# Optimization experiments

Measured on AMD Instinct MI355X. Metric: run time of the kernel, lower is better.

## Reference

```python
import jax, jax.numpy as jnp
import numpy as np

N = 50000      # nodes
E = 600000     # edges (avg degree 12)
IN = 128       # in_feat
HID = IN // 2  # 64
OUT = 128      # out_feat (must equal in_feat, see msg_linear)

# NOTE: the torch source uses nn.LeakyReLU(True): the positional arg is
# negative_slope, so slope == 1.0 (identity). We reproduce that faithfully.
NEG_SLOPE = 1.0

def leaky(v):
    return jnp.where(v >= 0, v, NEG_SLOPE * v)

def _linear_params(key, fan_in, fan_out):
    kw, kb = jax.random.split(key)
    bound = 1.0 / np.sqrt(fan_in)
    W = jax.random.uniform(kw, (fan_in, fan_out), jnp.float32, -bound, bound)
    b = jax.random.uniform(kb, (fan_out,), jnp.float32, -bound, bound)
    return W, b

def setup_inputs() -> dict:
    key = jax.random.key(0)
    ks = jax.random.split(key, 10)
    x = jax.random.normal(ks[0], (N, IN), jnp.float32)
    e = jax.random.normal(ks[1], (E, IN), jnp.float32)
    src = jax.random.randint(ks[2], (E,), 0, N, jnp.int64)
    dst = jax.random.randint(ks[3], (E,), 0, N, jnp.int64)
    W_nl1, b_nl1 = _linear_params(ks[4], IN, HID)    # node_linear1
    W_el, b_el = _linear_params(ks[5], IN, HID)      # edge_linear
    W1, b1 = _linear_params(ks[6], HID, HID)         # node_mlp layer 1
    W2, b2 = _linear_params(ks[7], HID, OUT)         # node_mlp layer 2
    W_nl2, b_nl2 = _linear_params(ks[8], IN, HID)    # node_linear2
    km, ke = jax.random.split(ks[9])
    W_ml, b_ml = _linear_params(km, IN, HID)         # msg_linear (in_feat==out_feat)
    W_em, b_em = _linear_params(ke, HID, OUT)        # edge_mlp layer
    return dict(x=x, e=e, src=src, dst=dst,
                W_nl1=W_nl1, b_nl1=b_nl1, W_el=W_el, b_el=b_el,
                W1=W1, b1=b1, W2=W2, b2=b2,
                W_nl2=W_nl2, b_nl2=b_nl2, W_ml=W_ml, b_ml=b_ml,
                W_em=W_em, b_em=b_em)

def reference(x, e, src, dst,
              W_nl1, b_nl1, W_el, b_el,
              W1, b1, W2, b2,
              W_nl2, b_nl2, W_ml, b_ml,
              W_em, b_em):
    # apply_edges: e' = node_mlp(node_linear1(x[src]) + edge_linear(e))
    z = x[src] @ W_nl1 + b_nl1 + e @ W_el + b_el            # [E, HID]
    e_new = leaky(leaky(z) @ W1 + b1) @ W2 + b2             # [E, OUT]
    # update_all(copy_e, sum): scatter-sum edge messages to destination nodes
    msg = jax.ops.segment_sum(e_new, dst, num_segments=N)   # [N, OUT]
    # x' = edge_mlp(node_linear2(x) + msg_linear(msg))
    h = leaky(x @ W_nl2 + b_nl2 + msg @ W_ml + b_ml)        # [N, HID]
    return h @ W_em + b_em                                  # [N, OUT]
```

## Files before the change

### kernel.cpp

```cpp
#include <hip/hip_runtime.h>

#define N_NODES 50000
#define N_EDGES 600000

typedef float v2f __attribute__((ext_vector_type(2)));

#define WF_PA   0
#define WF_UN   6400000
#define WI_CNT   9600000
#define WI_OFF   9650000
#define WI_CUR   9700000
#define WI_BSUM  9750000
#define WI_BOFF  9750256
#define WI_EPAIR 9750512
#define WF_T2   10950528
#define WF_BEG  10954624
#define WF_RH   10954752
#define WF_K1   10954816
#define WF_WAX  10958912
#define WF_WE   10975296
#define WF_R    10983488
#define WF_C2   10983616

#define NBLK_SCAN 196
#define NBLK_E    2344
#define NBLK_PT2  17
#define NBLK_K1   16
#define NBLK_WA   97
#define NBLK_PXA  391

__global__ __launch_bounds__(256) void f1_pret2_zero(
        const float* __restrict__ W2, const float* __restrict__ W_ml,
        const float* __restrict__ b1, const float* __restrict__ b2,
        float* __restrict__ T2, float* __restrict__ be_g,
        int* __restrict__ cnt) {
    int bid = blockIdx.x;
    if (bid < NBLK_PT2) {
        int idx = bid * 256 + threadIdx.x;
        if (idx < 4096) {
            int i = idx >> 6, j = idx & 63;
            float s = 0.f;
            for (int k = 0; k < 128; ++k) s += W2[i*128+k] * W_ml[k*64+j];
            T2[idx] = s;
        } else if (idx < 4224) {
            int j = idx - 4096;
            float s = b2[j];
            for (int k = 0; k < 64; ++k) s += b1[k] * W2[k*128+j];
            be_g[j] = s;
        }
    } else {
        int i = (bid - NBLK_PT2) * 256 + threadIdx.x;
        if (i < N_NODES) cnt[i] = 0;
    }
}

__global__ __launch_bounds__(256) void f2_prek1_hist(
        const float* __restrict__ W1, const float* __restrict__ T2,
        float* __restrict__ K1,
        const int* __restrict__ dst, int* __restrict__ cnt) {
    int bid = blockIdx.x;
    if (bid < NBLK_K1) {
        int idx = bid * 256 + threadIdx.x;
        int i = idx >> 6, j = idx & 63;
        float s = 0.f;
        for (int k = 0; k < 64; ++k) s += W1[i*64+k] * T2[k*64+j];
        K1[idx] = s;
    } else {
        int e = (bid - NBLK_K1) * 256 + threadIdx.x;
        if (e < N_EDGES) atomicAdd(&cnt[dst[e]], 1);
    }
}

__global__ __launch_bounds__(256) void f3_prewa_scana(
        const float* __restrict__ W_nl1, const float* __restrict__ W_el,
        const float* __restrict__ W_nl2, const float* __restrict__ K1,
        const float* __restrict__ b_nl1, const float* __restrict__ b_el,
        const float* __restrict__ be_g, const float* __restrict__ W_ml,
        float* __restrict__ WAX, float* __restrict__ WE,
        float* __restrict__ rh_g,
        const int* __restrict__ cnt, int* __restrict__ bsum) {
    int bid = blockIdx.x;
    if (bid < NBLK_WA) {
        int idx = bid * 256 + threadIdx.x;
        if (idx < 16384) {
            int i = idx >> 7, j = idx & 127;
            if (j < 64) {
                WAX[idx] = W_nl2[i*64+j];
            } else {
                float s = 0.f;
                for (int k = 0; k < 64; ++k) s += W_nl1[i*64+k] * K1[k*64+(j-64)];
                WAX[idx] = s;
            }
        } else if (idx < 24576) {
            int p = idx - 16384; int i = p >> 6, j = p & 63;
            float s = 0.f;
            for (int k = 0; k < 64; ++k) s += W_el[i*64+k] * K1[k*64+j];
            WE[p] = s;
        } else if (idx < 24640) {
            int t = idx - 24576;
            float s = 0.f;
            for (int k = 0; k < 64; ++k)  s += (b_nl1[k] + b_el[k]) * K1[k*64+t];
            for (int k = 0; k < 128; ++k) s += be_g[k] * W_ml[k*64+t];
            rh_g[t] = s;
        }
    } else {
        __shared__ int s[256];
        int blk = bid - NBLK_WA;
        int i = blk * 256 + threadIdx.x;
        int v = (i < N_NODES) ? cnt[i] : 0;
        s[threadIdx.x] = v;
        __syncthreads();
        for (int d = 128; d > 0; d >>= 1) {
            if (threadIdx.x < d) s[threadIdx.x] += s[threadIdx.x + d];
            __syncthreads();
        }
        if (threadIdx.x == 0) bsum[blk] = s[0];
    }
}

__global__ __launch_bounds__(256) void f4_prerc_scanb(
        const float* __restrict__ rh_g, const float* __restrict__ W_em,
        const float* __restrict__ b_nl2, const float* __restrict__ b_ml,
        const float* __restrict__ b_em,
        float* __restrict__ r, float* __restrict__ c2,
        const int* __restrict__ bsum, int* __restrict__ boff) {
    int t = threadIdx.x;
    if (blockIdx.x == 0) {
        if (t < 128) {
            float s = 0.f;
            for (int k = 0; k < 64; ++k) s += rh_g[k] * W_em[k*128+t];
            r[t] = s;
        } else {
            int j = t - 128;
            float s = b_em[j];
            for (int k = 0; k < 64; ++k) s += (b_nl2[k] + b_ml[k]) * W_em[k*128+j];
            c2[j] = s;
        }
    } else {
        __shared__ int s[256];
        int v = (t < NBLK_SCAN) ? bsum[t] : 0;
        s[t] = v;
        __syncthreads();
        for (int d = 1; d < 256; d <<= 1) {
            int tv = (t >= d) ? s[t - d] : 0;
            __syncthreads();
            s[t] += tv;
            __syncthreads();
        }
        if (t < NBLK_SCAN) boff[t] = s[t] - v;
    }
}

__global__ __launch_bounds__(256) void scan_c_kernel(const int* __restrict__ cnt,
                                                     const int* __restrict__ boff,
                                                     int* __restrict__ offs,
                                                     int* __restrict__ cursor) {
    __shared__ int s[256];
    int i = blockIdx.x * 256 + threadIdx.x;
    int t = threadIdx.x;
    int v = (i < N_NODES) ? cnt[i] : 0;
    s[t] = v;
    __syncthreads();
    for (int d = 1; d < 256; d <<= 1) {
        int tv = (t >= d) ? s[t - d] : 0;
        __syncthreads();
        s[t] += tv;
        __syncthreads();
    }
    if (i < N_NODES) {
        int ex = s[t] - v + boff[blockIdx.x];
        offs[i] = ex;
        cursor[i] = ex;
    }
}

__global__ __launch_bounds__(256) void f5_fill_pxa(
        const int* __restrict__ dst, const int* __restrict__ src,
        int* __restrict__ cursor, int2* __restrict__ epair,
        const float* __restrict__ x, const float* __restrict__ WAX,
        float* __restrict__ PA) {
    int bid = blockIdx.x;
    if (bid < NBLK_E) {
        int e = bid * 256 + threadIdx.x;
        if (e < N_EDGES) {
            int pos = atomicAdd(&cursor[dst[e]], 1);
            epair[pos] = make_int2(e, src[e]);
        }
        return;
    }
    __shared__ float As[32][133];
    __shared__ float Ws[32][128];
    int base = (bid - NBLK_E) * 128;
    int t = threadIdx.x;
    int cg = t & 15, rg = t >> 4;
    int c0 = cg * 8, r0 = rg * 8;

    float acc[8][8];
    #pragma unroll
    for (int i = 0; i < 8; ++i)
        #pragma unroll
        for (int j = 0; j < 8; ++j) acc[i][j] = 0.f;

    int arow0 = t >> 3;
    int akq   = t & 7;

    for (int k0 = 0; k0 < 128; k0 += 32) {
        __syncthreads();
        #pragma unroll
        for (int i = 0; i < 4; ++i) {
            int row = arow0 + i * 32;
            int n = base + row;
            float4 v = make_float4(0.f, 0.f, 0.f, 0.f);
            if (n < N_NODES)
                v = *(const float4*)&x[(size_t)n * 128 + k0 + akq * 4];
            As[akq * 4 + 0][row] = v.x;
            As[akq * 4 + 1][row] = v.y;
            As[akq * 4 + 2][row] = v.z;
            As[akq * 4 + 3][row] = v.w;
        }
        #pragma unroll
        for (int i = 0; i < 4; ++i) {
            int idx = t + i * 256;
            int row = idx >> 5, q4 = idx & 31;
            *(float4*)&Ws[row][q4 * 4] =
                *(const float4*)&WAX[(size_t)(k0 + row) * 128 + q4 * 4];
        }
        __syncthreads();
        #pragma unroll 8
        for (int k = 0; k < 32; ++k) {
            float a[8], w[8];
            *(float4*)&a[0] = *(const float4*)&As[k][r0];
            *(float4*)&a[4] = *(const float4*)&As[k][r0 + 4];
            *(float4*)&w[0] = *(const float4*)&Ws[k][c0];
            *(float4*)&w[4] = *(const float4*)&Ws[k][c0 + 4];
            #pragma unroll
            for (int i = 0; i < 8; ++i)
                #pragma unroll
                for (int jj = 0; jj < 8; ++jj)
                    acc[i][jj] += a[i] * w[jj];
        }
    }

    #pragma unroll
    for (int i = 0; i < 8; ++i) {
        int n = base + r0 + i;
        if (n < N_NODES) {
            *(float4*)&PA[(size_t)n * 128 + c0]     = *(float4*)&acc[i][0];
            *(float4*)&PA[(size_t)n * 128 + c0 + 4] = *(float4*)&acc[i][4];
        }
    }
}

__global__ __launch_bounds__(256) void gather_kernel(
        const float* __restrict__ PA, const float* __restrict__ ef,
        const int* __restrict__ cnt, const int* __restrict__ offs,
        const int2* __restrict__ epair, const float* __restrict__ WE,
        float* __restrict__ u) {
    int n    = (int)((blockIdx.x * 256 + threadIdx.x) >> 6);
    int lane = threadIdx.x & 63;
    if (n >= N_NODES) return;
    int off = offs[n], deg = cnt[n];
    int col2 = lane * 2;
    float a_val = PA[(size_t)n * 128 + lane];
    float apx = 0.f, ae0 = 0.f, ae1 = 0.f;
    for (int c0 = 0; c0 < deg; c0 += 64) {
        int j = c0 + lane;
        int2 p = make_int2(0, 0);
        if (j < deg) p = epair[off + j];
        int m = deg - c0; if (m > 64) m = 64;
        for (int j2 = 0; j2 < m; j2 += 8) {
            float xv[8]; v2f ev[8]; float msk[8];
            #pragma unroll
            for (int uu = 0; uu < 8; ++uu) {
                int jj = j2 + uu;
                int idx = (jj < m) ? jj : (m - 1);
                msk[uu] = (jj < m) ? 1.f : 0.f;
                int e_ = __shfl(p.x, idx);
                int s_ = __shfl(p.y, idx);
                xv[uu] = PA[(size_t)s_ * 128 + 64 + lane];
                ev[uu] = __builtin_nontemporal_load(
                            (const v2f*)(ef + (size_t)e_ * 128 + col2));
            }
            #pragma unroll
            for (int uu = 0; uu < 8; ++uu) {
                apx += msk[uu] * xv[uu];
                ae0 += msk[uu] * ev[uu][0];
                ae1 += msk[uu] * ev[uu][1];
            }
        }
    }
    const float* WEl = WE + lane;
    float pr0 = 0.f, pr1 = 0.f, pr2 = 0.f, pr3 = 0.f;
    for (int k0 = 0; k0 < 128; k0 += 8) {
        float wv[8], evv[8];
        #pragma unroll
        for (int uu = 0; uu < 8; ++uu) {
            int kk = k0 + uu;
            wv[uu]  = WEl[kk * 64];
            evv[uu] = __shfl((kk & 1) ? ae1 : ae0, kk >> 1);
        }
        pr0 += evv[0]*wv[0] + evv[4]*wv[4];
        pr1 += evv[1]*wv[1] + evv[5]*wv[5];
        pr2 += evv[2]*wv[2] + evv[6]*wv[6];
        pr3 += evv[3]*wv[3] + evv[7]*wv[7];
    }
    u[(size_t)n * 64 + lane] = a_val + apx + ((pr0 + pr1) + (pr2 + pr3));
}

__global__ __launch_bounds__(256) void gemm2_kernel(
        const float* __restrict__ u, const int* __restrict__ cnt,
        const float* __restrict__ W_em,
        const float* __restrict__ rvec, const float* __restrict__ c2,
        float* __restrict__ out) {
    __shared__ float UsT[64][69];
    __shared__ float Wem[64][128];
    int base = blockIdx.x * 64;
    int t = threadIdx.x;
    int cg = t & 15, rg = t >> 4;
    int c0 = cg * 8, r0 = rg * 4;

    #pragma unroll
    for (int i = 0; i < 4; ++i) {
        int idx = t + i * 256;
        int row = idx >> 4, kq = idx & 15;
        int n = base + row;
        float4 v = make_float4(0.f, 0.f, 0.f, 0.f);
        if (n < N_NODES) v = *(const float4*)&u[(size_t)n * 64 + kq * 4];
        UsT[kq * 4 + 0][row] = v.x;
        UsT[kq * 4 + 1][row] = v.y;
        UsT[kq * 4 + 2][row] = v.z;
        UsT[kq * 4 + 3][row] = v.w;
    }
    #pragma unroll
    for (int i = 0; i < 8; ++i) {
        int idx = t + i * 256;
        int row = idx >> 5, q4 = idx & 31;
        *(float4*)&Wem[row][q4 * 4] = *(const float4*)&W_em[(size_t)row * 128 + q4 * 4];
    }

    float4 rva = *(const float4*)&rvec[c0];
    float4 rvb = *(const float4*)&rvec[c0 + 4];
    float4 cva = *(const float4*)&c2[c0];
    float4 cvb = *(const float4*)&c2[c0 + 4];
    float acc[4][8];
    #pragma unroll
    for (int i = 0; i < 4; ++i) {
        int n = base + r0 + i;
        float dg = (n < N_NODES) ? (float)cnt[n] : 0.f;
        acc[i][0] = cva.x + dg * rva.x;  acc[i][1] = cva.y + dg * rva.y;
        acc[i][2] = cva.z + dg * rva.z;  acc[i][3] = cva.w + dg * rva.w;
        acc[i][4] = cvb.x + dg * rvb.x;  acc[i][5] = cvb.y + dg * rvb.y;
        acc[i][6] = cvb.z + dg * rvb.z;  acc[i][7] = cvb.w + dg * rvb.w;
    }
    __syncthreads();

    #pragma unroll 8
    for (int k = 0; k < 64; ++k) {
        float a[4], w[8];
        *(float4*)&a[0] = *(const float4*)&UsT[k][r0];
        *(float4*)&w[0] = *(const float4*)&Wem[k][c0];
        *(float4*)&w[4] = *(const float4*)&Wem[k][c0 + 4];
        #pragma unroll
        for (int i = 0; i < 4; ++i)
            #pragma unroll
            for (int j = 0; j < 8; ++j)
                acc[i][j] += a[i] * w[j];
    }

    #pragma unroll
    for (int i = 0; i < 4; ++i) {
        int n = base + r0 + i;
        if (n < N_NODES) {
            *(float4*)&out[(size_t)n * 128 + c0]     = *(float4*)&acc[i][0];
            *(float4*)&out[(size_t)n * 128 + c0 + 4] = *(float4*)&acc[i][4];
        }
    }
}

extern "C" void kernel_launch(void* const* d_in, const int* in_sizes, int n_in,
                              void* d_out, int out_size, void* d_ws, size_t ws_size,
                              hipStream_t stream) {
    const float* x     = (const float*)d_in[0];
    const float* ef    = (const float*)d_in[1];
    const int*   src   = (const int*)d_in[2];
    const int*   dst   = (const int*)d_in[3];
    const float* W_nl1 = (const float*)d_in[4];
    const float* b_nl1 = (const float*)d_in[5];
    const float* W_el  = (const float*)d_in[6];
    const float* b_el  = (const float*)d_in[7];
    const float* W1    = (const float*)d_in[8];
    const float* b1    = (const float*)d_in[9];
    const float* W2    = (const float*)d_in[10];
    const float* b2    = (const float*)d_in[11];
    const float* W_nl2 = (const float*)d_in[12];
    const float* b_nl2 = (const float*)d_in[13];
    const float* W_ml  = (const float*)d_in[14];
    const float* b_ml  = (const float*)d_in[15];
    const float* W_em  = (const float*)d_in[16];
    const float* b_em  = (const float*)d_in[17];

    int*   wsI = (int*)d_ws;
    float* wsF = (float*)d_ws;
    float* PA     = wsF + WF_PA;
    float* uN     = wsF + WF_UN;
    int*   cnt    = wsI + WI_CNT;
    int*   offs   = wsI + WI_OFF;
    int*   cursor = wsI + WI_CUR;
    int*   bsum   = wsI + WI_BSUM;
    int*   boff   = wsI + WI_BOFF;
    int2*  epair  = (int2*)(wsI + WI_EPAIR);
    float* T2   = wsF + WF_T2;
    float* be_g = wsF + WF_BEG;
    float* rh_g = wsF + WF_RH;
    float* K1   = wsF + WF_K1;
    float* WAX  = wsF + WF_WAX;
    float* WE   = wsF + WF_WE;
    float* r    = wsF + WF_R;
    float* c2   = wsF + WF_C2;

    f1_pret2_zero<<<NBLK_PT2 + NBLK_SCAN, 256, 0, stream>>>(
        W2, W_ml, b1, b2, T2, be_g, cnt);
    f2_prek1_hist<<<NBLK_K1 + NBLK_E, 256, 0, stream>>>(
        W1, T2, K1, dst, cnt);
    f3_prewa_scana<<<NBLK_WA + NBLK_SCAN, 256, 0, stream>>>(
        W_nl1, W_el, W_nl2, K1, b_nl1, b_el, be_g, W_ml, WAX, WE, rh_g,
        cnt, bsum);
    f4_prerc_scanb<<<2, 256, 0, stream>>>(
        rh_g, W_em, b_nl2, b_ml, b_em, r, c2, bsum, boff);
    scan_c_kernel<<<NBLK_SCAN, 256, 0, stream>>>(cnt, boff, offs, cursor);
    f5_fill_pxa<<<NBLK_E + NBLK_PXA, 256, 0, stream>>>(
        dst, src, cursor, epair, x, WAX, PA);

    gather_kernel<<<(N_NODES + 3) / 4, 256, 0, stream>>>(
        PA, ef, cnt, offs, epair, WE, uN);

    gemm2_kernel<<<(N_NODES + 63) / 64, 256, 0, stream>>>(
        uN, cnt, W_em, r, c2, (float*)d_out);
}
```

Baseline: 281.6 us.

## Move per-node WE projection out of gather into a tiled GEMM fused with output GEMM

The gather kernel now only sums edge features (as float4 loads split across two half-waves, each handling alternate edges) and projected source features. It writes the raw 128-wide edge sum and the partial node value to the workspace. The per-node 128x64 WE projection, previously done with shuffles and uncoalesced weight loads inside each wavefront, moves into a shared-memory tiled GEMM that is fused ahead of the existing W_em GEMM. This removes shuffle-heavy per-node matvec work from the latency-bound gather, at the cost of an extra 50000x128 intermediate written and read back through global memory.

Result: faster. 271.1 us (-3.7%).

```diff
diff --git a/kernel.cpp b/kernel.cpp
--- a/kernel.cpp
+++ b/kernel.cpp
@@ -4,30 +4,32 @@
 #define N_EDGES 600000
 
 typedef float v2f __attribute__((ext_vector_type(2)));
-
-#define WF_PA   0
-#define WF_UN   6400000
-#define WI_CNT   9600000
-#define WI_OFF   9650000
-#define WI_CUR   9700000
-#define WI_BSUM  9750000
-#define WI_BOFF  9750256
-#define WI_EPAIR 9750512
-#define WF_T2   10950528
-#define WF_BEG  10954624
-#define WF_RH   10954752
-#define WF_K1   10954816
-#define WF_WAX  10958912
-#define WF_WE   10975296
-#define WF_R    10983488
-#define WF_C2   10983616
+typedef float v4f __attribute__((ext_vector_type(4)));
+
+#define WF_PA    0
+#define WF_ES    6400000
+#define WF_UP    12800000
+#define WI_CNT   16000000
+#define WI_OFF   16050000
+#define WI_CUR   16100000
+#define WI_BSUM  16150000
+#define WI_BOFF  16150256
+#define WI_EPAIR 16150512
+#define WF_T2    17350528
+#define WF_BEG   17354624
+#define WF_RH    17354752
+#define WF_K1    17354816
+#define WF_WAX   17358912
+#define WF_WE    17375296
+#define WF_R     17383488
+#define WF_C2    17383616
 
 #define NBLK_SCAN 196
 #define NBLK_E    2344
 #define NBLK_PT2  17
 #define NBLK_K1   16
 #define NBLK_WA   97
-#define NBLK_PXA  391
+#define NBLK_PA   391
 
 __global__ __launch_bounds__(256) void f1_pret2_zero(
         const float* __restrict__ W2, const float* __restrict__ W_ml,
@@ -174,7 +176,7 @@
     }
 }
 
-__global__ __launch_bounds__(256) void f5_fill_pxa(
+__global__ __launch_bounds__(256) void f5_fill_pa(
         const int* __restrict__ dst, const int* __restrict__ src,
         int* __restrict__ cursor, int2* __restrict__ epair,
         const float* __restrict__ x, const float* __restrict__ WAX,
@@ -254,125 +256,171 @@
 __global__ __launch_bounds__(256) void gather_kernel(
         const float* __restrict__ PA, const float* __restrict__ ef,
         const int* __restrict__ cnt, const int* __restrict__ offs,
-        const int2* __restrict__ epair, const float* __restrict__ WE,
-        float* __restrict__ u) {
+        const int2* __restrict__ epair,
+        float* __restrict__ es, float* __restrict__ u_part) {
     int n    = (int)((blockIdx.x * 256 + threadIdx.x) >> 6);
     int lane = threadIdx.x & 63;
     if (n >= N_NODES) return;
     int off = offs[n], deg = cnt[n];
-    int col2 = lane * 2;
-    float a_val = PA[(size_t)n * 128 + lane];
-    float apx = 0.f, ae0 = 0.f, ae1 = 0.f;
+    int half = lane >> 5;
+    int hl   = lane & 31;
+    int ce4  = hl * 4;
+    int cp2  = hl * 2;
+    float ae0 = 0.f, ae1 = 0.f, ae2 = 0.f, ae3 = 0.f;
+    float ap0 = 0.f, ap1 = 0.f;
     for (int c0 = 0; c0 < deg; c0 += 64) {
         int j = c0 + lane;
         int2 p = make_int2(0, 0);
         if (j < deg) p = epair[off + j];
         int m = deg - c0; if (m > 64) m = 64;
         for (int j2 = 0; j2 < m; j2 += 8) {
-            float xv[8]; v2f ev[8]; float msk[8];
+            v4f ev[4]; v2f pv[4]; float msk[4];
             #pragma unroll
-            for (int uu = 0; uu < 8; ++uu) {
-                int jj = j2 + uu;
+            for (int q = 0; q < 4; ++q) {
+                int jj = j2 + q * 2 + half;
                 int idx = (jj < m) ? jj : (m - 1);
-                msk[uu] = (jj < m) ? 1.f : 0.f;
+                msk[q] = (jj < m) ? 1.f : 0.f;
                 int e_ = __shfl(p.x, idx);
                 int s_ = __shfl(p.y, idx);
-                xv[uu] = PA[(size_t)s_ * 128 + 64 + lane];
-                ev[uu] = __builtin_nontemporal_load(
-                            (const v2f*)(ef + (size_t)e_ * 128 + col2));
+                ev[q] = __builtin_nontemporal_load(
+                            (const v4f*)(ef + (size_t)e_ * 128 + ce4));
+                pv[q] = *(const v2f*)(PA + (size_t)s_ * 128 + 64 + cp2);
             }
             #pragma unroll
-            for (int uu = 0; uu < 8; ++uu) {
-                apx += msk[uu] * xv[uu];
-                ae0 += msk[uu] * ev[uu][0];
-                ae1 += msk[uu] * ev[uu][1];
+            for (int q = 0; q < 4; ++q) {
+                ae0 += msk[q] * ev[q][0];
+                ae1 += msk[q] * ev[q][1];
+                ae2 += msk[q] * ev[q][2];
+                ae3 += msk[q] * ev[q][3];
+                ap0 += msk[q] * pv[q][0];
+                ap1 += msk[q] * pv[q][1];
             }
         }
     }
-    const float* WEl = WE + lane;
-    float pr0 = 0.f, pr1 = 0.f, pr2 = 0.f, pr3 = 0.f;
-    for (int k0 = 0; k0 < 128; k0 += 8) {
-        float wv[8], evv[8];
-        #pragma unroll
-        for (int uu = 0; uu < 8; ++uu) {
-            int kk = k0 + uu;
-            wv[uu]  = WEl[kk * 64];
-            evv[uu] = __shfl((kk & 1) ? ae1 : ae0, kk >> 1);
-        }
-        pr0 += evv[0]*wv[0] + evv[4]*wv[4];
-        pr1 += evv[1]*wv[1] + evv[5]*wv[5];
-        pr2 += evv[2]*wv[2] + evv[6]*wv[6];
-        pr3 += evv[3]*wv[3] + evv[7]*wv[7];
-    }
-    u[(size_t)n * 64 + lane] = a_val + apx + ((pr0 + pr1) + (pr2 + pr3));
-}
-
-__global__ __launch_bounds__(256) void gemm2_kernel(
-        const float* __restrict__ u, const int* __restrict__ cnt,
+    ae0 += __shfl_xor(ae0, 32);
+    ae1 += __shfl_xor(ae1, 32);
+    ae2 += __shfl_xor(ae2, 32);
+    ae3 += __shfl_xor(ae3, 32);
+    ap0 += __shfl_xor(ap0, 32);
+    ap1 += __shfl_xor(ap1, 32);
+    if (half == 0) {
+        *(float4*)&es[(size_t)n * 128 + ce4] = make_float4(ae0, ae1, ae2, ae3);
+    } else {
+        float2 av = *(const float2*)&PA[(size_t)n * 128 + cp2];
+        *(float2*)&u_part[(size_t)n * 64 + cp2] = make_float2(av.x + ap0, av.y + ap1);
+    }
+}
+
+__global__ __launch_bounds__(256) void gemm12_kernel(
+        const float* __restrict__ es, const float* __restrict__ u_part,
+        const float* __restrict__ WE, const int* __restrict__ cnt,
         const float* __restrict__ W_em,
         const float* __restrict__ rvec, const float* __restrict__ c2,
         float* __restrict__ out) {
-    __shared__ float UsT[64][69];
-    __shared__ float Wem[64][128];
+    __shared__ union SM {
+        struct { float As[32][69]; float Ws[32][64]; } a;
+        struct { float UsT[64][69]; float Wem[64][128]; } b;
+    } sm;
     int base = blockIdx.x * 64;
     int t = threadIdx.x;
     int cg = t & 15, rg = t >> 4;
-    int c0 = cg * 8, r0 = rg * 4;
-
+
+    int c0a = cg * 4, r0a = rg * 4;
+    float accA[4][4];
     #pragma unroll
     for (int i = 0; i < 4; ++i) {
-        int idx = t + i * 256;
-        int row = idx >> 4, kq = idx & 15;
-        int n = base + row;
-        float4 v = make_float4(0.f, 0.f, 0.f, 0.f);
-        if (n < N_NODES) v = *(const float4*)&u[(size_t)n * 64 + kq * 4];
-        UsT[kq * 4 + 0][row] = v.x;
-        UsT[kq * 4 + 1][row] = v.y;
-        UsT[kq * 4 + 2][row] = v.z;
-        UsT[kq * 4 + 3][row] = v.w;
-    }
+        int n = base + r0a + i;
+        float4 pv = make_float4(0.f, 0.f, 0.f, 0.f);
+        if (n < N_NODES) pv = *(const float4*)&u_part[(size_t)n * 64 + c0a];
+        accA[i][0] = pv.x; accA[i][1] = pv.y; accA[i][2] = pv.z; accA[i][3] = pv.w;
+    }
+
+    for (int k0 = 0; k0 < 128; k0 += 32) {
+        __syncthreads();
+        #pragma unroll
+        for (int i = 0; i < 2; ++i) {
+            int idx = t + i * 256;
+            int row = idx >> 3, kq = idx & 7;
+            int n = base + row;
+            float4 v = make_float4(0.f, 0.f, 0.f, 0.f);
+            if (n < N_NODES)
+                v = *(const float4*)&es[(size_t)n * 128 + k0 + kq * 4];
+            sm.a.As[kq * 4 + 0][row] = v.x;
+            sm.a.As[kq * 4 + 1][row] = v.y;
+            sm.a.As[kq * 4 + 2][row] = v.z;
+            sm.a.As[kq * 4 + 3][row] = v.w;
+        }
+        #pragma unroll
+        for (int i = 0; i < 2; ++i) {
+            int idx = t + i * 256;
+            int row = idx >> 4, q4 = idx & 15;
+            *(float4*)&sm.a.Ws[row][q4 * 4] =
+                *(const float4*)&WE[(size_t)(k0 + row) * 64 + q4 * 4];
+        }
+        __syncthreads();
+        #pragma unroll 8
+        for (int k = 0; k < 32; ++k) {
+            float a[4], w[4];
+            *(float4*)&a[0] = *(const float4*)&sm.a.As[k][r0a];
+            *(float4*)&w[0] = *(const float4*)&sm.a.Ws[k][c0a];
+            #pragma unroll
+            for (int i = 0; i < 4; ++i)
+                #pragma unroll
+                for (int j = 0; j < 4; ++j)
+                    accA[i][j] += a[i] * w[j];
+        }
+    }
+
+    __syncthreads();
+    #pragma unroll
+    for (int j = 0; j < 4; ++j)
+        #pragma unroll
+        for (int i = 0; i < 4; ++i)
+            sm.b.UsT[c0a + j][r0a + i] = accA[i][j];
     #pragma unroll
     for (int i = 0; i < 8; ++i) {
         int idx = t + i * 256;
         int row = idx >> 5, q4 = idx & 31;
-        *(float4*)&Wem[row][q4 * 4] = *(const float4*)&W_em[(size_t)row * 128 + q4 * 4];
-    }
-
-    float4 rva = *(const float4*)&rvec[c0];
-    float4 rvb = *(const float4*)&rvec[c0 + 4];
-    float4 cva = *(const float4*)&c2[c0];
-    float4 cvb = *(const float4*)&c2[c0 + 4];
-    float acc[4][8];
+        *(float4*)&sm.b.Wem[row][q4 * 4] =
+            *(const float4*)&W_em[(size_t)row * 128 + q4 * 4];
+    }
+
+    int c0b = cg * 8, r0b = rg * 4;
+    float4 rva = *(const float4*)&rvec[c0b];
+    float4 rvb = *(const float4*)&rvec[c0b + 4];
+    float4 cva = *(const float4*)&c2[c0b];
+    float4 cvb = *(const float4*)&c2[c0b + 4];
+    float accB[4][8];
     #pragma unroll
     for (int i = 0; i < 4; ++i) {
-        int n = base + r0 + i;
+        int n = base + r0b + i;
         float dg = (n < N_NODES) ? (float)cnt[n] : 0.f;
-        acc[i][0] = cva.x + dg * rva.x;  acc[i][1] = cva.y + dg * rva.y;
-        acc[i][2] = cva.z + dg * rva.z;  acc[i][3] = cva.w + dg * rva.w;
-        acc[i][4] = cvb.x + dg * rvb.x;  acc[i][5] = cvb.y + dg * rvb.y;
-        acc[i][6] = cvb.z + dg * rvb.z;  acc[i][7] = cvb.w + dg * rvb.w;
+        accB[i][0] = cva.x + dg * rva.x;  accB[i][1] = cva.y + dg * rva.y;
+        accB[i][2] = cva.z + dg * rva.z;  accB[i][3] = cva.w + dg * rva.w;
+        accB[i][4] = cvb.x + dg * rvb.x;  accB[i][5] = cvb.y + dg * rvb.y;
+        accB[i][6] = cvb.z + dg * rvb.z;  accB[i][7] = cvb.w + dg * rvb.w;
     }
     __syncthreads();
 
     #pragma unroll 8
     for (int k = 0; k < 64; ++k) {
         float a[4], w[8];
-        *(float4*)&a[0] = *(const float4*)&UsT[k][r0];
-        *(float4*)&w[0] = *(const float4*)&Wem[k][c0];
-        *(float4*)&w[4] = *(const float4*)&Wem[k][c0 + 4];
+        *(float4*)&a[0] = *(const float4*)&sm.b.UsT[k][r0b];
+        *(float4*)&w[0] = *(const float4*)&sm.b.Wem[k][c0b];
+        *(float4*)&w[4] = *(const float4*)&sm.b.Wem[k][c0b + 4];
         #pragma unroll
         for (int i = 0; i < 4; ++i)
             #pragma unroll
             for (int j = 0; j < 8; ++j)
-                acc[i][j] += a[i] * w[j];
+                accB[i][j] += a[i] * w[j];
     }
 
     #pragma unroll
     for (int i = 0; i < 4; ++i) {
-        int n = base + r0 + i;
+        int n = base + r0b + i;
         if (n < N_NODES) {
-            *(float4*)&out[(size_t)n * 128 + c0]     = *(float4*)&acc[i][0];
-            *(float4*)&out[(size_t)n * 128 + c0 + 4] = *(float4*)&acc[i][4];
+            *(float4*)&out[(size_t)n * 128 + c0b]     = *(float4*)&accB[i][0];
+            *(float4*)&out[(size_t)n * 128 + c0b + 4] = *(float4*)&accB[i][4];
         }
     }
 }
@@ -402,7 +450,8 @@
     int*   wsI = (int*)d_ws;
     float* wsF = (float*)d_ws;
     float* PA     = wsF + WF_PA;
-    float* uN     = wsF + WF_UN;
+    float* es     = wsF + WF_ES;
+    float* u_part = wsF + WF_UP;
     int*   cnt    = wsI + WI_CNT;
     int*   offs   = wsI + WI_OFF;
     int*   cursor = wsI + WI_CUR;
@@ -420,20 +469,19 @@
 
     f1_pret2_zero<<<NBLK_PT2 + NBLK_SCAN, 256, 0, stream>>>(
         W2, W_ml, b1, b2, T2, be_g, cnt);
-    f2_prek1_hist<<<NBLK_K1 + NBLK_E, 256, 0, stream>>>(
-        W1, T2, K1, dst, cnt);
+    f2_prek1_hist<<<NBLK_K1 + NBLK_E, 256, 0, stream>>>(W1, T2, K1, dst, cnt);
     f3_prewa_scana<<<NBLK_WA + NBLK_SCAN, 256, 0, stream>>>(
         W_nl1, W_el, W_nl2, K1, b_nl1, b_el, be_g, W_ml, WAX, WE, rh_g,
         cnt, bsum);
     f4_prerc_scanb<<<2, 256, 0, stream>>>(
         rh_g, W_em, b_nl2, b_ml, b_em, r, c2, bsum, boff);
     scan_c_kernel<<<NBLK_SCAN, 256, 0, stream>>>(cnt, boff, offs, cursor);
-    f5_fill_pxa<<<NBLK_E + NBLK_PXA, 256, 0, stream>>>(
+    f5_fill_pa<<<NBLK_E + NBLK_PA, 256, 0, stream>>>(
         dst, src, cursor, epair, x, WAX, PA);
 
     gather_kernel<<<(N_NODES + 3) / 4, 256, 0, stream>>>(
-        PA, ef, cnt, offs, epair, WE, uN);
-
-    gemm2_kernel<<<(N_NODES + 63) / 64, 256, 0, stream>>>(
-        uN, cnt, W_em, r, c2, (float*)d_out);
-}
+        PA, ef, cnt, offs, epair, es, u_part);
+
+    gemm12_kernel<<<(N_NODES + 63) / 64, 256, 0, stream>>>(
+        es, u_part, WE, cnt, W_em, r, c2, (float*)d_out);
+}
```
